# Optimization experiments

Measured on AMD Instinct MI355X. Metric: run time of the kernel, lower is better.

The kernel has to match this reference:

```python
import jax, jax.numpy as jnp
import numpy as np

Q_DIM = 1024
K_DIM = 1024
V_DIM = 1024
ATTEN_DIM = 1024
NUM_HEADS = 16
HEAD_DIM = ATTEN_DIM // NUM_HEADS
B, L = 4, 2048


def setup_inputs() -> dict:
    key = jax.random.key(0)
    ks = jax.random.split(key, 11)
    s = 0.02
    return {
        "query": jax.random.normal(ks[0], (B, L, Q_DIM), dtype=jnp.float32),
        "key":   jax.random.normal(ks[1], (B, L, K_DIM), dtype=jnp.float32),
        "value": jax.random.normal(ks[2], (B, L, V_DIM), dtype=jnp.float32),
        "Wq": jax.random.normal(ks[3], (Q_DIM, ATTEN_DIM), dtype=jnp.float32) * s,
        "bq": jnp.zeros((ATTEN_DIM,), dtype=jnp.float32),
        "Wk": jax.random.normal(ks[4], (K_DIM, ATTEN_DIM), dtype=jnp.float32) * s,
        "bk": jnp.zeros((ATTEN_DIM,), dtype=jnp.float32),
        "Wv": jax.random.normal(ks[5], (V_DIM, ATTEN_DIM), dtype=jnp.float32) * s,
        "bv": jnp.zeros((ATTEN_DIM,), dtype=jnp.float32),
        "Wo": jax.random.normal(ks[6], (ATTEN_DIM, V_DIM), dtype=jnp.float32) * s,
        "bo": jnp.zeros((V_DIM,), dtype=jnp.float32),
    }


def reference(query, key, value, Wq, bq, Wk, bk, Wv, bv, Wo, bo):
    # QKV projections
    q = query @ Wq + bq        # [B, L, A]
    k = key   @ Wk + bk        # [B, L, A]
    v = value @ Wv + bv        # [B, L, A]
    # split heads: [B, L, H, D]
    def split_heads(x):
        return x.reshape(x.shape[:-1] + (NUM_HEADS, HEAD_DIM))
    q, k, v = split_heads(q), split_heads(k), split_heads(v)
    scale = 1.0 / (HEAD_DIM ** 0.5)
    # scores: [B, H, Lq, Lk]
    scores = jnp.einsum("bqhd,bkhd->bhqk", q, k) * scale
    attn = jax.nn.softmax(scores, axis=-1)
    out = jnp.einsum("bhqk,bkhd->bqhd", attn, v)  # [B, Lq, H, D]
    out = out.reshape(out.shape[0], out.shape[1], ATTEN_DIM)
    return out @ Wo + bo
```

## Files before the change

### kernel.cpp

```cpp
#include <hip/hip_runtime.h>
#include <stdint.h>

#define L_SEQ 2048
#define BATCH 4
#define ADIM  1024
#define NH    16
#define HD    64
#define KT    128

typedef __attribute__((ext_vector_type(8))) short bf16x8;
typedef __attribute__((ext_vector_type(4))) float f32x4;

__device__ __forceinline__ short f2bf(float f) {
    union { float f; unsigned u; } x; x.f = f;
    unsigned r = x.u + 0x7fffu + ((x.u >> 16) & 1u);
    return (short)(r >> 16);
}

__device__ __forceinline__ void async_ld16(void* lds, const void* g) {
    __builtin_amdgcn_global_load_lds(
        (const __attribute__((address_space(1))) void*)g,
        (__attribute__((address_space(3))) void*)lds, 16, 0, 0);
}

__global__ void cvt3_kernel(const float* __restrict__ s0, const float* __restrict__ s1,
                            const float* __restrict__ s2, short* __restrict__ dst, int n4) {
    int i = blockIdx.x * blockDim.x + threadIdx.x;
    if (i >= n4) return;
    int z = blockIdx.y;
    const float* src = (z == 0) ? s0 : (z == 1) ? s1 : s2;
    float4 v = reinterpret_cast<const float4*>(src)[i];
    short4 s;
    s.x = f2bf(v.x); s.y = f2bf(v.y); s.z = f2bf(v.z); s.w = f2bf(v.w);
    reinterpret_cast<short4*>(dst + (size_t)z * (BATCH * L_SEQ * ADIM))[i] = s;
}

__global__ void transpose4_kernel(const float* __restrict__ W0, const float* __restrict__ W1,
                                  const float* __restrict__ W2, const float* __restrict__ W3,
                                  short* __restrict__ outb) {
    __shared__ float t[32][33];
    int z = blockIdx.z;
    const float* in = (z == 0) ? W0 : (z == 1) ? W1 : (z == 2) ? W2 : W3;
    short* out = outb + (size_t)z * (ADIM * ADIM);
    int x  = blockIdx.x * 32 + threadIdx.x;
    int y0 = blockIdx.y * 32 + threadIdx.y;
#pragma unroll
    for (int j = 0; j < 4; ++j)
        t[threadIdx.y + 8 * j][threadIdx.x] = in[(y0 + 8 * j) * 1024 + x];
    __syncthreads();
    int x2 = blockIdx.y * 32 + threadIdx.x;
    int y2 = blockIdx.x * 32 + threadIdx.y;
#pragma unroll
    for (int j = 0; j < 4; ++j)
        out[(y2 + 8 * j) * 1024 + x2] = f2bf(t[threadIdx.x][threadIdx.y + 8 * j]);
}

__device__ __forceinline__ void gemm_core(const short* __restrict__ A,
                                          const short* __restrict__ BT,
                                          const float* __restrict__ bias,
                                          void* __restrict__ Cout,
                                          int mode, float scalemul) {
    const int K = 1024, N = 1024;
    __shared__ __align__(16) short As[128 * 32];
    __shared__ __align__(16) short Bs[128 * 32];
    int tid = threadIdx.x;
    int wave = tid >> 6, lane = tid & 63, quad = lane >> 4, l16 = lane & 15;
    int wm = wave & 1, wn = wave >> 1;
    int m0 = blockIdx.y * 128, n0 = blockIdx.x * 128;
    f32x4 acc[4][4] = {};

    int row = tid >> 2, ck = tid & 3;
    const short* gA0 = A  + (size_t)(m0 + row) * K + ck * 8;
    const short* gA1 = gA0 + (size_t)64 * K;
    const short* gB0 = BT + (size_t)(n0 + row) * K + ck * 8;
    const short* gB1 = gB0 + (size_t)64 * K;
    short* lA0 = As + tid * 8;  short* lA1 = As + tid * 8 + 2048;
    short* lB0 = Bs + tid * 8;  short* lB1 = Bs + tid * 8 + 2048;

    for (int kb = 0; kb < K; kb += 32) {
        async_ld16(lA0, gA0); async_ld16(lA1, gA1);
        async_ld16(lB0, gB0); async_ld16(lB1, gB1);
        gA0 += 32; gA1 += 32; gB0 += 32; gB1 += 32;
        __syncthreads();
        bf16x8 af[4], bf[4];
#pragma unroll
        for (int mt = 0; mt < 4; ++mt)
            af[mt] = *(const bf16x8*)&As[(wm * 64 + mt * 16 + l16) * 32 + quad * 8];
#pragma unroll
        for (int nt = 0; nt < 4; ++nt)
            bf[nt] = *(const bf16x8*)&Bs[(wn * 64 + nt * 16 + l16) * 32 + quad * 8];
#pragma unroll
        for (int mt = 0; mt < 4; ++mt)
#pragma unroll
            for (int nt = 0; nt < 4; ++nt)
                acc[mt][nt] = __builtin_amdgcn_mfma_f32_16x16x32_bf16(
                    af[mt], bf[nt], acc[mt][nt], 0, 0, 0);
        __syncthreads();
    }

    if (mode == 0) {
#pragma unroll
        for (int nt = 0; nt < 4; ++nt) {
            int col = n0 + wn * 64 + nt * 16 + l16;
            float bv = bias[col];
#pragma unroll
            for (int mt = 0; mt < 4; ++mt)
#pragma unroll
                for (int r = 0; r < 4; ++r) {
                    int rw = m0 + wm * 64 + mt * 16 + quad * 4 + r;
                    ((short*)Cout)[(size_t)rw * N + col] = f2bf((acc[mt][nt][r] + bv) * scalemul);
                }
        }
    } else if (mode == 1) {
#pragma unroll
        for (int nt = 0; nt < 4; ++nt) {
            int col = n0 + wn * 64 + nt * 16 + l16;
            float bv = bias[col];
            int h = col >> 6, d = col & 63;
#pragma unroll
            for (int mt = 0; mt < 4; ++mt)
#pragma unroll
                for (int r = 0; r < 4; ++r) {
                    int rw = m0 + wm * 64 + mt * 16 + quad * 4 + r;
                    int b = rw >> 11, lk = rw & 2047;
                    ((short*)Cout)[(((size_t)b * NH + h) * HD + d) * L_SEQ + lk] =
                        f2bf(acc[mt][nt][r] + bv);
                }
        }
    } else {
#pragma unroll
        for (int nt = 0; nt < 4; ++nt) {
            int col = n0 + wn * 64 + nt * 16 + l16;
            float bv = bias[col];
#pragma unroll
            for (int mt = 0; mt < 4; ++mt)
#pragma unroll
                for (int r = 0; r < 4; ++r) {
                    int rw = m0 + wm * 64 + mt * 16 + quad * 4 + r;
                    ((float*)Cout)[(size_t)rw * N + col] = acc[mt][nt][r] + bv;
                }
        }
    }
}

__global__ __launch_bounds__(256)
void gemm_one(const short* __restrict__ A, const short* __restrict__ BT,
              const float* __restrict__ bias, void* __restrict__ Cout,
              int mode, float scalemul) {
    gemm_core(A, BT, bias, Cout, mode, scalemul);
}

__global__ __launch_bounds__(256)
void qkv_gemm(const short* __restrict__ Xbase, const short* __restrict__ WTbase,
              const float* __restrict__ bq, const float* __restrict__ bk,
              const float* __restrict__ bv,
              short* __restrict__ Qb, short* __restrict__ Kb, short* __restrict__ VTout,
              float qscale) {
    int z = blockIdx.z;
    const short* A  = Xbase + (size_t)z * (BATCH * L_SEQ * ADIM);
    const short* BT = WTbase + (size_t)z * (ADIM * ADIM);
    const float* bias = (z == 0) ? bq : (z == 1) ? bk : bv;
    void* out = (z == 0) ? (void*)Qb : (z == 1) ? (void*)Kb : (void*)VTout;
    int mode = (z == 2) ? 1 : 0;
    float sm = (z == 0) ? qscale : 1.0f;
    gemm_core(A, BT, bias, out, mode, sm);
}

#define KS_OFF 0
#define VS_OFF (KT * 72)
#define PS_OFF (VS_OFF + 64 * 136)
#define LDS_TOT (PS_OFF + 4 * 16 * 136)

__global__ __launch_bounds__(256)
void attn_kernel(const short* __restrict__ Qb, const short* __restrict__ Kb,
                 const short* __restrict__ VT, short* __restrict__ Oout) {
    __shared__ __align__(16) short lds[LDS_TOT];
    int tid = threadIdx.x;
    int wave = tid >> 6, lane = tid & 63, quad = lane >> 4, l16 = lane & 15;
    int h = blockIdx.y, b = blockIdx.z;
    int q0 = blockIdx.x * 64 + wave * 16;

    int qrow = b * L_SEQ + q0 + l16;
    bf16x8 qlo = *(const bf16x8*)&Qb[(size_t)qrow * ADIM + h * HD + quad * 8];
    bf16x8 qhi = *(const bf16x8*)&Qb[(size_t)qrow * ADIM + h * HD + 32 + quad * 8];

    const short* Kbase = Kb + (size_t)b * L_SEQ * ADIM + h * HD;
    const short* Vbase = VT + ((size_t)(b * NH + h) * HD) * L_SEQ;
    const short* gp[9];
    int lof[9], gst[9];
#pragma unroll
    for (int s = 0; s < 9; ++s) {
        int idx = tid + s * 256;
        if (idx < 1152) {
            int row = idx / 9, ck = idx - row * 9;
            gp[s] = Kbase + (size_t)row * ADIM + ck * 8;
            lof[s] = KS_OFF + idx * 8;
            gst[s] = KT * ADIM;
        } else {
            int j = idx - 1152; if (j >= 1088) j = 0;
            int row = j / 17, ck = j - row * 17;
            gp[s] = Vbase + (size_t)row * L_SEQ + ck * 8;
            lof[s] = VS_OFF + j * 8;
            gst[s] = KT;
        }
    }

    f32x4 lpart = {};
    f32x4 o[4] = {};
    short* psw = lds + PS_OFF + wave * 16 * 136;

    for (int kb = 0; kb < L_SEQ; kb += KT) {
        __syncthreads();
#pragma unroll
        for (int s = 0; s < 8; ++s) {
            async_ld16(lds + lof[s], gp[s]);
            gp[s] += gst[s];
        }
        if (tid < 192) async_ld16(lds + lof[8], gp[8]);
        gp[8] += gst[8];
        __syncthreads();

        f32x4 sv[8];
#pragma unroll
        for (int nt = 0; nt < 8; ++nt) {
            const short* kr = lds + KS_OFF + (nt * 16 + l16) * 72;
            bf16x8 k0 = *(const bf16x8*)&kr[quad * 8];
            bf16x8 k1 = *(const bf16x8*)&kr[32 + quad * 8];
            f32x4 z = {};
            z = __builtin_amdgcn_mfma_f32_16x16x32_bf16(qlo, k0, z, 0, 0, 0);
            z = __builtin_amdgcn_mfma_f32_16x16x32_bf16(qhi, k1, z, 0, 0, 0);
            sv[nt] = z;
        }

#pragma unroll
        for (int nt = 0; nt < 8; ++nt)
#pragma unroll
            for (int r = 0; r < 4; ++r) {
                float p = __builtin_amdgcn_exp2f(sv[nt][r]);
                sv[nt][r] = p;
                lpart[r] += p;
            }

#pragma unroll
        for (int nt = 0; nt < 8; nt += 2)
#pragma unroll
            for (int r = 0; r < 4; ++r) {
                int a = (quad * 4 + r) * 136 + nt * 16 + l16;
#if __has_builtin(__builtin_amdgcn_cvt_pk_bf16_f32)
                auto pk = __builtin_amdgcn_cvt_pk_bf16_f32(sv[nt][r], sv[nt + 1][r]);
                unsigned u; __builtin_memcpy(&u, &pk, 4);
                psw[a]      = (short)(u & 0xffffu);
                psw[a + 16] = (short)(u >> 16);
#else
                psw[a]      = f2bf(sv[nt][r]);
                psw[a + 16] = f2bf(sv[nt + 1][r]);
#endif
            }

        bf16x8 pf[4];
#pragma unroll
        for (int c = 0; c < 4; ++c)
            pf[c] = *(const bf16x8*)&psw[l16 * 136 + c * 32 + quad * 8];
#pragma unroll
        for (int nt = 0; nt < 4; ++nt) {
            const short* vr = lds + VS_OFF + (nt * 16 + l16) * 136;
#pragma unroll
            for (int c = 0; c < 4; ++c) {
                bf16x8 vf = *(const bf16x8*)&vr[c * 32 + quad * 8];
                o[nt] = __builtin_amdgcn_mfma_f32_16x16x32_bf16(pf[c], vf, o[nt], 0, 0, 0);
            }
        }
    }

    float l_i[4];
#pragma unroll
    for (int r = 0; r < 4; ++r) {
        float v = lpart[r];
        v += __shfl_xor(v, 1);
        v += __shfl_xor(v, 2);
        v += __shfl_xor(v, 4);
        v += __shfl_xor(v, 8);
        l_i[r] = v;
    }
#pragma unroll
    for (int r = 0; r < 4; ++r) {
        float inv = __builtin_amdgcn_rcpf(l_i[r]);
        int row = b * L_SEQ + q0 + quad * 4 + r;
#pragma unroll
        for (int nt = 0; nt < 4; ++nt) {
            int col = h * HD + nt * 16 + l16;
            Oout[(size_t)row * ADIM + col] = f2bf(o[nt][r] * inv);
        }
    }
}

extern "C" void kernel_launch(void* const* d_in, const int* in_sizes, int n_in,
                              void* d_out, int out_size, void* d_ws, size_t ws_size,
                              hipStream_t stream) {
    const float* query = (const float*)d_in[0];
    const float* keyp  = (const float*)d_in[1];
    const float* value = (const float*)d_in[2];
    const float* Wq = (const float*)d_in[3];
    const float* bq = (const float*)d_in[4];
    const float* Wk = (const float*)d_in[5];
    const float* bk = (const float*)d_in[6];
    const float* Wv = (const float*)d_in[7];
    const float* bv = (const float*)d_in[8];
    const float* Wo = (const float*)d_in[9];
    const float* bo = (const float*)d_in[10];

    const float QSCALE = 0.125f * 1.44269504f;
    const size_t MB = 1ull << 20;
    const int n4 = (BATCH * L_SEQ * ADIM) / 4;
    char* w = (char*)d_ws;
    dim3 tblk(32, 8);
    dim3 gemm_grid(ADIM / 128, (BATCH * L_SEQ) / 128);
    dim3 attn_grid(L_SEQ / 64, NH, BATCH);

    if (ws_size >= 104 * MB) {
        short* X0  = (short*)(w);
        short* WT  = (short*)(w + 48 * MB);
        short* VT  = (short*)(w + 56 * MB);
        short* Kb  = (short*)(w + 72 * MB);
        short* Qb  = (short*)(w + 88 * MB);
        short* AO  = X0;

        cvt3_kernel<<<dim3(n4 / 256, 3), 256, 0, stream>>>(query, keyp, value, X0, n4);
        transpose4_kernel<<<dim3(32, 32, 4), tblk, 0, stream>>>(Wq, Wk, Wv, Wo, WT);
        qkv_gemm<<<dim3(ADIM / 128, (BATCH * L_SEQ) / 128, 3), 256, 0, stream>>>(
            X0, WT, bq, bk, bv, Qb, Kb, VT, QSCALE);
        attn_kernel<<<attn_grid, 256, 0, stream>>>(Qb, Kb, VT, AO);
        gemm_one<<<gemm_grid, 256, 0, stream>>>(AO, WT + (size_t)3 * ADIM * ADIM, bo,
                                                d_out, 2, 1.0f);
    } else {
        short* X0  = (short*)(w);
        short* WT  = (short*)(w + 16 * MB);
        short* VT  = (short*)(w + 24 * MB);
        short* Kb  = (short*)(w + 40 * MB);
        short* Qb  = (short*)(w + 56 * MB);

        transpose4_kernel<<<dim3(32, 32, 4), tblk, 0, stream>>>(Wq, Wk, Wv, Wo, WT);
        cvt3_kernel<<<dim3(n4 / 256, 1), 256, 0, stream>>>(query, query, query, X0, n4);
        gemm_one<<<gemm_grid, 256, 0, stream>>>(X0, WT, bq, Qb, 0, QSCALE);
        cvt3_kernel<<<dim3(n4 / 256, 1), 256, 0, stream>>>(keyp, keyp, keyp, X0, n4);
        gemm_one<<<gemm_grid, 256, 0, stream>>>(X0, WT + (size_t)ADIM * ADIM, bk, Kb, 0, 1.0f);
        cvt3_kernel<<<dim3(n4 / 256, 1), 256, 0, stream>>>(value, value, value, X0, n4);
        gemm_one<<<gemm_grid, 256, 0, stream>>>(X0, WT + (size_t)2 * ADIM * ADIM, bv, VT, 1, 1.0f);
        attn_kernel<<<attn_grid, 256, 0, stream>>>(Qb, Kb, VT, X0);
        gemm_one<<<gemm_grid, 256, 0, stream>>>(X0, WT + (size_t)3 * ADIM * ADIM, bo,
                                                d_out, 2, 1.0f);
    }
}
```

Before: 401.3 us.

## Double queries per attention wave and vectorize V-transpose stores via LDS

The attention kernel now has each wave handle 32 query rows (two 16-row tiles) instead of 16. Each K/V tile loaded into LDS is reused twice as much, and the grid halves, which cuts the global-to-LDS traffic of K and V. The V projection epilogue now stages the transposed output through shared memory so it can write 16-byte vector stores instead of scattered 2-byte stores. In exchange, register pressure in the attention kernel roughly doubles for the accumulators. The P staging buffer is also reused serially for the two query tiles, which adds LDS round-trips.

New measurement: 405.1 us. About the same (+0.9%).

```diff
diff --git a/kernel.cpp b/kernel.cpp
--- a/kernel.cpp
+++ b/kernel.cpp
@@ -61,8 +61,9 @@
                                           void* __restrict__ Cout,
                                           int mode, float scalemul) {
     const int K = 1024, N = 1024;
-    __shared__ __align__(16) short As[128 * 32];
-    __shared__ __align__(16) short Bs[128 * 32];
+    __shared__ __align__(16) short smem[8192];
+    short* As = smem;
+    short* Bs = smem + 4096;
     int tid = threadIdx.x;
     int wave = tid >> 6, lane = tid & 63, quad = lane >> 4, l16 = lane & 15;
     int wm = wave & 1, wn = wave >> 1;
@@ -112,20 +113,30 @@
                 }
         }
     } else if (mode == 1) {
+        short* tsc = smem + wave * 1152;
+        int cr = lane >> 2, sg = lane & 3;
 #pragma unroll
         for (int nt = 0; nt < 4; ++nt) {
             int col = n0 + wn * 64 + nt * 16 + l16;
             float bv = bias[col];
-            int h = col >> 6, d = col & 63;
-#pragma unroll
-            for (int mt = 0; mt < 4; ++mt)
-#pragma unroll
-                for (int r = 0; r < 4; ++r) {
-                    int rw = m0 + wm * 64 + mt * 16 + quad * 4 + r;
-                    int b = rw >> 11, lk = rw & 2047;
-                    ((short*)Cout)[(((size_t)b * NH + h) * HD + d) * L_SEQ + lk] =
-                        f2bf(acc[mt][nt][r] + bv);
-                }
+#pragma unroll
+            for (int mt = 0; mt < 4; ++mt) {
+                short4 p;
+                p.x = f2bf(acc[mt][nt][0] + bv);
+                p.y = f2bf(acc[mt][nt][1] + bv);
+                p.z = f2bf(acc[mt][nt][2] + bv);
+                p.w = f2bf(acc[mt][nt][3] + bv);
+                *(short4*)&tsc[l16 * 72 + mt * 16 + quad * 4] = p;
+            }
+            bf16x8 v0 = *(const bf16x8*)&tsc[cr * 72 + sg * 16];
+            bf16x8 v1 = *(const bf16x8*)&tsc[cr * 72 + sg * 16 + 8];
+            int colg = n0 + wn * 64 + nt * 16 + cr;
+            int hh = colg >> 6, dd = colg & 63;
+            int rwb = m0 + wm * 64 + sg * 16;
+            int bb = rwb >> 11, lk = rwb & 2047;
+            short* dst = (short*)Cout + (((size_t)bb * NH + hh) * HD + dd) * L_SEQ + lk;
+            *(bf16x8*)dst = v0;
+            *(bf16x8*)(dst + 8) = v1;
         }
     } else {
 #pragma unroll
@@ -171,18 +182,22 @@
 #define PS_OFF (VS_OFF + 64 * 136)
 #define LDS_TOT (PS_OFF + 4 * 16 * 136)
 
-__global__ __launch_bounds__(256)
+__global__ __launch_bounds__(256, 3)
 void attn_kernel(const short* __restrict__ Qb, const short* __restrict__ Kb,
                  const short* __restrict__ VT, short* __restrict__ Oout) {
     __shared__ __align__(16) short lds[LDS_TOT];
     int tid = threadIdx.x;
     int wave = tid >> 6, lane = tid & 63, quad = lane >> 4, l16 = lane & 15;
     int h = blockIdx.y, b = blockIdx.z;
-    int q0 = blockIdx.x * 64 + wave * 16;
-
-    int qrow = b * L_SEQ + q0 + l16;
-    bf16x8 qlo = *(const bf16x8*)&Qb[(size_t)qrow * ADIM + h * HD + quad * 8];
-    bf16x8 qhi = *(const bf16x8*)&Qb[(size_t)qrow * ADIM + h * HD + 32 + quad * 8];
+    int q0 = blockIdx.x * 128 + wave * 32;
+
+    int qrowA = b * L_SEQ + q0 + l16;
+    const short* qpA = Qb + (size_t)qrowA * ADIM + h * HD;
+    bf16x8 qloA = *(const bf16x8*)&qpA[quad * 8];
+    bf16x8 qhiA = *(const bf16x8*)&qpA[32 + quad * 8];
+    const short* qpB = qpA + (size_t)16 * ADIM;
+    bf16x8 qloB = *(const bf16x8*)&qpB[quad * 8];
+    bf16x8 qhiB = *(const bf16x8*)&qpB[32 + quad * 8];
 
     const short* Kbase = Kb + (size_t)b * L_SEQ * ADIM + h * HD;
     const short* Vbase = VT + ((size_t)(b * NH + h) * HD) * L_SEQ;
@@ -205,8 +220,8 @@
         }
     }
 
-    f32x4 lpart = {};
-    f32x4 o[4] = {};
+    f32x4 lpA = {}, lpB = {};
+    f32x4 oA[4] = {}, oB[4] = {};
     short* psw = lds + PS_OFF + wave * 16 * 136;
 
     for (int kb = 0; kb < L_SEQ; kb += KT) {
@@ -220,25 +235,28 @@
         gp[8] += gst[8];
         __syncthreads();
 
-        f32x4 sv[8];
+        f32x4 sA[8], sB[8];
 #pragma unroll
         for (int nt = 0; nt < 8; ++nt) {
             const short* kr = lds + KS_OFF + (nt * 16 + l16) * 72;
             bf16x8 k0 = *(const bf16x8*)&kr[quad * 8];
             bf16x8 k1 = *(const bf16x8*)&kr[32 + quad * 8];
-            f32x4 z = {};
-            z = __builtin_amdgcn_mfma_f32_16x16x32_bf16(qlo, k0, z, 0, 0, 0);
-            z = __builtin_amdgcn_mfma_f32_16x16x32_bf16(qhi, k1, z, 0, 0, 0);
-            sv[nt] = z;
+            f32x4 zA = {}, zB = {};
+            zA = __builtin_amdgcn_mfma_f32_16x16x32_bf16(qloA, k0, zA, 0, 0, 0);
+            zB = __builtin_amdgcn_mfma_f32_16x16x32_bf16(qloB, k0, zB, 0, 0, 0);
+            zA = __builtin_amdgcn_mfma_f32_16x16x32_bf16(qhiA, k1, zA, 0, 0, 0);
+            zB = __builtin_amdgcn_mfma_f32_16x16x32_bf16(qhiB, k1, zB, 0, 0, 0);
+            sA[nt] = zA; sB[nt] = zB;
         }
 
 #pragma unroll
         for (int nt = 0; nt < 8; ++nt)
 #pragma unroll
             for (int r = 0; r < 4; ++r) {
-                float p = __builtin_amdgcn_exp2f(sv[nt][r]);
-                sv[nt][r] = p;
-                lpart[r] += p;
+                float pA = __builtin_amdgcn_exp2f(sA[nt][r]);
+                float pB = __builtin_amdgcn_exp2f(sB[nt][r]);
+                sA[nt][r] = pA; sB[nt][r] = pB;
+                lpA[r] += pA; lpB[r] += pB;
             }
 
 #pragma unroll
@@ -247,49 +265,67 @@
             for (int r = 0; r < 4; ++r) {
                 int a = (quad * 4 + r) * 136 + nt * 16 + l16;
 #if __has_builtin(__builtin_amdgcn_cvt_pk_bf16_f32)
-                auto pk = __builtin_amdgcn_cvt_pk_bf16_f32(sv[nt][r], sv[nt + 1][r]);
+                auto pk = __builtin_amdgcn_cvt_pk_bf16_f32(sA[nt][r], sA[nt + 1][r]);
                 unsigned u; __builtin_memcpy(&u, &pk, 4);
                 psw[a]      = (short)(u & 0xffffu);
                 psw[a + 16] = (short)(u >> 16);
 #else
-                psw[a]      = f2bf(sv[nt][r]);
-                psw[a + 16] = f2bf(sv[nt + 1][r]);
+                psw[a]      = f2bf(sA[nt][r]);
+                psw[a + 16] = f2bf(sA[nt + 1][r]);
 #endif
             }
-
-        bf16x8 pf[4];
+        bf16x8 pfA[4];
 #pragma unroll
         for (int c = 0; c < 4; ++c)
-            pf[c] = *(const bf16x8*)&psw[l16 * 136 + c * 32 + quad * 8];
+            pfA[c] = *(const bf16x8*)&psw[l16 * 136 + c * 32 + quad * 8];
+
+#pragma unroll
+        for (int nt = 0; nt < 8; nt += 2)
+#pragma unroll
+            for (int r = 0; r < 4; ++r) {
+                int a = (quad * 4 + r) * 136 + nt * 16 + l16;
+#if __has_builtin(__builtin_amdgcn_cvt_pk_bf16_f32)
+                auto pk = __builtin_amdgcn_cvt_pk_bf16_f32(sB[nt][r], sB[nt + 1][r]);
+                unsigned u; __builtin_memcpy(&u, &pk, 4);
+                psw[a]      = (short)(u & 0xffffu);
+                psw[a + 16] = (short)(u >> 16);
+#else
+                psw[a]      = f2bf(sB[nt][r]);
+                psw[a + 16] = f2bf(sB[nt + 1][r]);
+#endif
+            }
+        bf16x8 pfB[4];
+#pragma unroll
+        for (int c = 0; c < 4; ++c)
+            pfB[c] = *(const bf16x8*)&psw[l16 * 136 + c * 32 + quad * 8];
+
 #pragma unroll
         for (int nt = 0; nt < 4; ++nt) {
             const short* vr = lds + VS_OFF + (nt * 16 + l16) * 136;
 #pragma unroll
             for (int c = 0; c < 4; ++c) {
                 bf16x8 vf = *(const bf16x8*)&vr[c * 32 + quad * 8];
-                o[nt] = __builtin_amdgcn_mfma_f32_16x16x32_bf16(pf[c], vf, o[nt], 0, 0, 0);
-            }
-        }
-    }
-
-    float l_i[4];
+                oA[nt] = __builtin_amdgcn_mfma_f32_16x16x32_bf16(pfA[c], vf, oA[nt], 0, 0, 0);
+                oB[nt] = __builtin_amdgcn_mfma_f32_16x16x32_bf16(pfB[c], vf, oB[nt], 0, 0, 0);
+            }
+        }
+    }
+
 #pragma unroll
     for (int r = 0; r < 4; ++r) {
-        float v = lpart[r];
-        v += __shfl_xor(v, 1);
-        v += __shfl_xor(v, 2);
-        v += __shfl_xor(v, 4);
-        v += __shfl_xor(v, 8);
-        l_i[r] = v;
-    }
-#pragma unroll
-    for (int r = 0; r < 4; ++r) {
-        float inv = __builtin_amdgcn_rcpf(l_i[r]);
-        int row = b * L_SEQ + q0 + quad * 4 + r;
+        float vA = lpA[r], vB = lpB[r];
+        vA += __shfl_xor(vA, 1); vB += __shfl_xor(vB, 1);
+        vA += __shfl_xor(vA, 2); vB += __shfl_xor(vB, 2);
+        vA += __shfl_xor(vA, 4); vB += __shfl_xor(vB, 4);
+        vA += __shfl_xor(vA, 8); vB += __shfl_xor(vB, 8);
+        float invA = __builtin_amdgcn_rcpf(vA);
+        float invB = __builtin_amdgcn_rcpf(vB);
+        int rowA = b * L_SEQ + q0 + quad * 4 + r;
 #pragma unroll
         for (int nt = 0; nt < 4; ++nt) {
             int col = h * HD + nt * 16 + l16;
-            Oout[(size_t)row * ADIM + col] = f2bf(o[nt][r] * inv);
+            Oout[(size_t)rowA * ADIM + col] = f2bf(oA[nt][r] * invA);
+            Oout[(size_t)(rowA + 16) * ADIM + col] = f2bf(oB[nt][r] * invB);
         }
     }
 }
@@ -315,7 +351,7 @@
     char* w = (char*)d_ws;
     dim3 tblk(32, 8);
     dim3 gemm_grid(ADIM / 128, (BATCH * L_SEQ) / 128);
-    dim3 attn_grid(L_SEQ / 64, NH, BATCH);
+    dim3 attn_grid(L_SEQ / 128, NH, BATCH);
 
     if (ws_size >= 104 * MB) {
         short* X0  = (short*)(w);
```
